# Optimization experiments

Hardware: AMD Instinct MI355X
Metric: run time of the kernel (lower is better)

Reference implementation:

```python
import jax, jax.numpy as jnp
import numpy as np

STRIDES = [8, 16, 32]
FMP = [(320, 320), (160, 160), (80, 80)]  # H,W per level for 2560x2560 input
NUM_CLASSES = 80
TOPK = 1000
CONF_THRESH = 0.05
NMS_THRESH = 0.6
CLASS_OFFSET = 8192.0  # > max coordinate; separates classes for class-aware NMS


def setup_inputs() -> dict:
    key = jax.random.key(0)
    ks = jax.random.split(key, 9)
    d = {}
    for i, (h, w) in enumerate(FMP):
        M = h * w
        d[f"obj{i}"] = jax.random.normal(ks[3 * i], (M, 1), jnp.float32)
        d[f"cls{i}"] = jax.random.normal(ks[3 * i + 1], (M, NUM_CLASSES), jnp.float32)
        d[f"reg{i}"] = jax.random.normal(ks[3 * i + 2], (M, 4), jnp.float32) * 0.5
    return d


def _anchors(level):
    h, w = FMP[level]
    ys, xs = jnp.meshgrid(jnp.arange(h), jnp.arange(w), indexing='ij')
    xy = jnp.stack([xs, ys], axis=-1).reshape(-1, 2).astype(jnp.float32) + 0.5
    return xy * STRIDES[level]  # [M, 2]


def _decode_boxes(anchors, regs, stride):
    ctr = anchors + regs[..., :2] * stride
    wh = jnp.exp(regs[..., 2:]) * stride
    return jnp.concatenate([ctr - 0.5 * wh, ctr + 0.5 * wh], axis=-1)


def _level_topk(obj, cls_, reg, level):
    # fused score: sqrt(sigmoid(obj) * sigmoid(cls)), flattened over [M*C]
    scores = jnp.sqrt(jax.nn.sigmoid(obj) * jax.nn.sigmoid(cls_)).reshape(-1)
    top_s, top_i = jax.lax.top_k(scores, TOPK)
    valid = top_s > CONF_THRESH  # original filters; we mask (jit-friendly)
    anchor_idx = top_i // NUM_CLASSES
    labels = top_i % NUM_CLASSES
    boxes = _decode_boxes(_anchors(level)[anchor_idx], reg[anchor_idx], STRIDES[level])
    return top_s, labels, boxes, valid


def _iou_matrix(b):
    # b: [N,4] -> pairwise IoU [N,N]
    area = (b[:, 2] - b[:, 0]) * (b[:, 3] - b[:, 1])
    lt = jnp.maximum(b[:, None, :2], b[None, :, :2])
    rb = jnp.minimum(b[:, None, 2:], b[None, :, 2:])
    wh = jnp.clip(rb - lt, 0.0)
    inter = wh[..., 0] * wh[..., 1]
    return inter / (area[:, None] + area[None, :] - inter + 1e-9)


def _multiclass_nms(boxes, scores, labels, valid):
    N = scores.shape[0]
    order = jnp.argsort(-scores)
    boxes = boxes[order]
    scores = scores[order]
    labels = labels[order]
    valid = valid[order]
    # class-aware NMS via coordinate offset trick
    off_boxes = boxes + (labels.astype(jnp.float32) * CLASS_OFFSET)[:, None]
    iou = _iou_matrix(off_boxes)
    idx = jnp.arange(N)

    def body(i, keep):
        sup = (iou[i] > NMS_THRESH) & (idx > i)
        return jnp.where(keep[i], keep & ~sup, keep)

    keep = jax.lax.fori_loop(0, N, body, valid)
    return boxes, scores, labels, keep


def reference(obj0, cls0, reg0, obj1, cls1, reg1, obj2, cls2, reg2):
    objs, clss, regs = [obj0, obj1, obj2], [cls0, cls1, cls2], [reg0, reg1, reg2]
    S, L, B, V = [], [], [], []
    for lvl in range(3):
        s, l, b, v = _level_topk(objs[lvl], clss[lvl], regs[lvl], lvl)
        S.append(s); L.append(l); B.append(b); V.append(v)
    scores = jnp.concatenate(S)
    labels = jnp.concatenate(L)
    boxes = jnp.concatenate(B)
    valid = jnp.concatenate(V)
    boxes, scores, labels, keep = _multiclass_nms(boxes, scores, labels, valid)
    return boxes, scores, labels, keep
```

## Files before the change

kernel.cpp:

```cpp
#include <hip/hip_runtime.h>

typedef unsigned int u32;
typedef unsigned long long u64;

#define NCLS 80
#define NTOT 3000
#define CAND_CAP 4096
#define NBLK 525

#define WS_HIST   0
#define WS_CNT    3072
#define WS_DONEA  3200
#define WS_DONEB  3328
#define WS_DONEC  3456
#define WS_CAND   4096
#define WS_SEL    102400

#define PB_HALF    0x3F000000u
#define PB_QUARTER 0x3E800000u

__device__ __forceinline__ float sigm(float x) {
#pragma clang fp contract(off)
    return 1.0f / (1.0f + expf(-x));
}

__device__ __forceinline__ u32 cload32(const u32* p) {
    return __hip_atomic_load(p, __ATOMIC_RELAXED, __HIP_MEMORY_SCOPE_AGENT);
}
__device__ __forceinline__ u64 cload64(const u64* p) {
    return __hip_atomic_load(p, __ATOMIC_RELAXED, __HIP_MEMORY_SCOPE_AGENT);
}
__device__ __forceinline__ void cstore64(u64* p, u64 v) {
    __hip_atomic_store(p, v, __ATOMIC_RELAXED, __HIP_MEMORY_SCOPE_AGENT);
}
__device__ __forceinline__ void arrive(u32* flag) {
    __hip_atomic_fetch_add(flag, 1u, __ATOMIC_RELEASE, __HIP_MEMORY_SCOPE_AGENT);
}
__device__ __forceinline__ void wait_for(u32* flag, u32 target) {
    int it = 0;
    while (__hip_atomic_load(flag, __ATOMIC_RELAXED, __HIP_MEMORY_SCOPE_AGENT) < target
           && it++ < (1 << 24)) {
        __builtin_amdgcn_s_sleep(8);
    }
    (void)__hip_atomic_load(flag, __ATOMIC_ACQUIRE, __HIP_MEMORY_SCOPE_AGENT);
}

__device__ __forceinline__ void block_map(int b, int& L, int& m0) {
    if (b < 400)      { L = 0; m0 = b * 256; }
    else if (b < 500) { L = 1; m0 = (b - 400) * 256; }
    else              { L = 2; m0 = (b - 500) * 256; }
}

__global__ __launch_bounds__(256) void fused_kernel(
    const float* __restrict__ o0, const float* __restrict__ c0, const float* __restrict__ r0,
    const float* __restrict__ o1, const float* __restrict__ c1, const float* __restrict__ r1,
    const float* __restrict__ o2, const float* __restrict__ c2, const float* __restrict__ r2,
    float* __restrict__ out,
    u32* __restrict__ whist, u32* __restrict__ wcnt,
    u32* __restrict__ doneA, u32* __restrict__ doneB, u32* __restrict__ doneC,
    u64* __restrict__ wcand, u64* __restrict__ wsel) {
#pragma clang fp contract(off)
    __shared__ u64 smem64[4096];
    int tid = threadIdx.x;
    int b = (int)blockIdx.x;
    u32 lane = (u32)(tid & 63);
    int L, m0; block_map(b, L, m0);
    const float* obj = (L == 0) ? o0 : ((L == 1) ? o1 : o2);
    const float* cls = (L == 0) ? c0 : ((L == 1) ? c1 : c2);
    const float4* cls4 = (const float4*)cls;

    {
        u32* h = (u32*)smem64;
        u32* alist = h + 8 * 257;
        float* slist = (float*)(alist + 256);
        u32* nshp = (u32*)(slist + 256);
        for (int k = tid; k < 8 * 257; k += 256) h[k] = 0u;
        if (tid == 0) *nshp = 0u;
        __syncthreads();
        float so = sigm(obj[m0 + tid]);
        bool pass = __float_as_uint(so) >= PB_HALF;
        u64 mask = __ballot(pass);
        u32 pc = (u32)__popcll(mask);
        u32 wbase = 0;
        if (lane == 0 && pc) wbase = atomicAdd(nshp, pc);
        wbase = (u32)__shfl((int)wbase, 0);
        if (pass) {
            u32 off = (u32)__popcll(mask & ((1ull << lane) - 1ull));
            alist[wbase + off] = (u32)tid;
            slist[wbase + off] = so;
        }
        __syncthreads();
        int n = (int)*nshp;
        u32 rep = (u32)(tid & 7);
        for (int i = tid; i < n * 20; i += 256) {
            int j = i / 20, k = i - j * 20;
            int a = m0 + (int)alist[j];
            float soj = slist[j];
            float4 v = cls4[a * 20 + k];
            float vv[4] = {v.x, v.y, v.z, v.w};
#pragma unroll
            for (int q = 0; q < 4; ++q) {
                float p = soj * sigm(vv[q]);
                u32 pb = __float_as_uint(p);
                if (pb >= PB_HALF) {
                    u32 bin = min((pb >> 15) - 0x7E00u, 255u);
                    atomicAdd(&h[rep * 257 + bin], 1u);
                }
            }
        }
        __syncthreads();
        if (tid < 256) {
            u32 s = 0;
            for (int r = 0; r < 8; ++r) s += h[r * 257 + tid];
            if (s) atomicAdd(&whist[L * 256 + tid], s);
        }
    }
    __syncthreads();
    if (tid == 0) { arrive(doneA); wait_for(doneA, NBLK); }
    __syncthreads();

    {
        u32* sh = (u32*)smem64;
        u32* alist = sh + 256;
        float* slist = (float*)(alist + 256);
        int* cutbin = (int*)(slist + 256);
        u32* thrsh = (u32*)(cutbin + 1);
        u32* nshp = thrsh + 1;
        if (tid == 0) { *cutbin = -1; *nshp = 0u; }
        sh[tid] = cload32(&whist[L * 256 + tid]);
        __syncthreads();
        for (int off = 1; off < 256; off <<= 1) {
            u32 v = (tid + off < 256) ? sh[tid + off] : 0u;
            __syncthreads();
            sh[tid] += v;
            __syncthreads();
        }
        if (sh[tid] >= 1000u) atomicMax(cutbin, tid);
        __syncthreads();
        if (tid == 0) {
            *thrsh = (*cutbin >= 0) ? (PB_HALF + ((u32)*cutbin << 15)) - 0x8000u
                                    : PB_QUARTER;
        }
        __syncthreads();
        u32 thr = *thrsh;
        float so = sigm(obj[m0 + tid]);
        bool pass = __float_as_uint(so) >= thr;
        u64 mask = __ballot(pass);
        u32 pc = (u32)__popcll(mask);
        u32 wbase = 0;
        if (lane == 0 && pc) wbase = atomicAdd(nshp, pc);
        wbase = (u32)__shfl((int)wbase, 0);
        if (pass) {
            u32 off = (u32)__popcll(mask & ((1ull << lane) - 1ull));
            alist[wbase + off] = (u32)tid;
            slist[wbase + off] = so;
        }
        __syncthreads();
        int n = (int)*nshp;
        for (int i = tid; i < n * 20; i += 256) {
            int j = i / 20, k = i - j * 20;
            int a = m0 + (int)alist[j];
            float soj = slist[j];
            float4 v = cls4[a * 20 + k];
            float vv[4] = {v.x, v.y, v.z, v.w};
#pragma unroll
            for (int q = 0; q < 4; ++q) {
                float p = soj * sigm(vv[q]);
                u32 pb = __float_as_uint(p);
                bool emit = (pb >= thr);
                u64 em = __ballot(emit);
                if (em) {
                    u32 cw = (u32)__popcll(em);
                    u32 base = 0;
                    if (lane == 0) base = atomicAdd(&wcnt[L], cw);
                    base = (u32)__shfl((int)base, 0);
                    if (emit) {
                        u32 slot = base + (u32)__popcll(em & ((1ull << lane) - 1ull));
                        if (slot < CAND_CAP) {
                            float s = sqrtf(p);
                            u32 sb = __float_as_uint(s);
                            u32 idx = (u32)(a * NCLS + (k * 4 + q));
                            cstore64(&wcand[L * CAND_CAP + slot],
                                     ((u64)(sb ^ 0xFFFFFFFFu) << 32) | idx);
                        }
                    }
                }
            }
        }
    }
    __syncthreads();
    if (tid == 0) arrive(doneB);

    if (b < 48) {
        if (tid == 0) wait_for(doneB, NBLK);
        __syncthreads();
        u64* s = smem64;
        int RL = b >> 4, part = b & 15;
        int n = (int)min(cload32(&wcnt[RL]), (u32)CAND_CAP);
        if (part * 256 < n) {
            for (int j = tid; j < n; j += 256) s[j] = cload64(&wcand[RL * CAND_CAP + j]);
            __syncthreads();
            int i = part * 256 + tid;
            if (i < n) {
                u64 mykey = s[i];
                int rank = 0;
#pragma unroll 4
                for (int j = 0; j < n; ++j) rank += (s[j] < mykey);
                if (rank < 1000) cstore64(&wsel[RL * 1000 + rank], mykey);
            }
        }
        __syncthreads();
        if (tid == 0) arrive(doneC);
        return;
    }

    if (b >= 128) return;
    {
        int c = b - 48;
        u64* k = smem64;
        u64* ckey = smem64 + 3000;
        u32* cidx = (u32*)(smem64 + 3256);
        u32* ncp = (u32*)(smem64 + 3384);
        if (tid == 0) { *ncp = 0u; wait_for(doneC, 48); }
        __syncthreads();
        for (int i = tid; i < NTOT; i += 256) {
            u64 S = cload64(&wsel[i]);
            u64 key = (S & 0xFFFFFFFF00000000ull) | (u32)i;
            k[i] = key;
            u32 idx = (u32)S;
            if ((int)(idx % NCLS) == c) {
                u32 p = atomicAdd(ncp, 1u);
                if (p < 256) { ckey[p] = key; cidx[p] = idx; }
            }
        }
        __syncthreads();
        int nc = (int)min(*ncp, 256u);
        int g = -1, r = 0;
        u32 myidx = 0;
        u64 mykey = 0;
        if (tid < nc) {
            mykey = ckey[tid];
            myidx = cidx[tid];
            for (int j = 0; j < nc; ++j) r += (ckey[j] < mykey);
            int t = (int)(u32)mykey;
            int ML = t / 1000;
            g = t - ML * 1000;
            for (int O = 0; O < 3; ++O) {
                if (O == ML) continue;
                int lo = 0, hi = 1000;
                while (lo < hi) {
                    int mid = (lo + hi) >> 1;
                    if (k[O * 1000 + mid] < mykey) lo = mid + 1; else hi = mid;
                }
                g += lo;
            }
        }
        __syncthreads();
        u32* garr = (u32*)smem64;
        u32* invp = (u32*)(smem64 + 64);
        float* bx = (float*)(smem64 + 512);
        if (tid < nc) {
            garr[tid] = (u32)g;
            invp[r] = (u32)tid;
            int t = (int)(u32)mykey;
            int ML = t / 1000;
            u32 bits = (u32)(mykey >> 32) ^ 0xFFFFFFFFu;
            float score = __uint_as_float(bits);
            int m = (int)(myidx / NCLS);
            int w = (ML == 0) ? 320 : ((ML == 1) ? 160 : 80);
            float st = (ML == 0) ? 8.0f : ((ML == 1) ? 16.0f : 32.0f);
            const float* reg = (ML == 0) ? r0 : ((ML == 1) ? r1 : r2);
            int x = m % w, y = m / w;
            float rv0 = reg[m * 4 + 0], rv1 = reg[m * 4 + 1];
            float rv2 = reg[m * 4 + 2], rv3 = reg[m * 4 + 3];
            float ax = ((float)x + 0.5f) * st;
            float ay = ((float)y + 0.5f) * st;
            float cx = ax + rv0 * st;
            float cy = ay + rv1 * st;
            float bw = expf(rv2) * st;
            float bh = expf(rv3) * st;
            float hx = 0.5f * bw, hy = 0.5f * bh;
            float x1 = cx - hx, y1 = cy - hy, x2 = cx + hx, y2 = cy + hy;
            out[g * 4 + 0] = x1; out[g * 4 + 1] = y1;
            out[g * 4 + 2] = x2; out[g * 4 + 3] = y2;
            out[12000 + g] = score;
            out[15000 + g] = (float)c;
            float off = (float)c * 8192.0f;
            bx[tid * 4 + 0] = x1 + off; bx[tid * 4 + 1] = y1 + off;
            bx[tid * 4 + 2] = x2 + off; bx[tid * 4 + 3] = y2 + off;
        }
        __syncthreads();
        if (tid < 64) {
            int K = (nc + 63) >> 6;
            u32 alive = 0;
            for (int kk = 0; kk < K; ++kk) {
                int p = tid + (kk << 6);
                if (p < nc) {
                    u32 bits = (u32)(ckey[invp[p]] >> 32) ^ 0xFFFFFFFFu;
                    if (__uint_as_float(bits) > 0.05f) alive |= (1u << kk);
                }
            }
            for (int a = 0; a < nc; ++a) {
                u32 owner = (u32)__shfl((int)alive, a & 63);
                if ((owner >> (a >> 6)) & 1u) {
                    int ra = (int)invp[a];
                    float a0 = bx[ra * 4 + 0], a1 = bx[ra * 4 + 1];
                    float a2 = bx[ra * 4 + 2], a3 = bx[ra * 4 + 3];
                    float areaA = (a2 - a0) * (a3 - a1);
                    for (int kk = (a >> 6); kk < K; ++kk) {
                        int p = tid + (kk << 6);
                        if (p > a && p < nc && ((alive >> kk) & 1u)) {
                            int rp = (int)invp[p];
                            float b0 = bx[rp * 4 + 0], b1 = bx[rp * 4 + 1];
                            float b2 = bx[rp * 4 + 2], b3 = bx[rp * 4 + 3];
                            float areaB = (b2 - b0) * (b3 - b1);
                            float ltx = fmaxf(a0, b0), lty = fmaxf(a1, b1);
                            float rbx = fminf(a2, b2), rby = fminf(a3, b3);
                            float wx = fmaxf(rbx - ltx, 0.0f), wy = fmaxf(rby - lty, 0.0f);
                            float inter = wx * wy;
                            float denom = ((areaA + areaB) - inter) + 1e-9f;
                            float iou = inter / denom;
                            if (iou > 0.6f) alive &= ~(1u << kk);
                        }
                    }
                }
            }
            for (int kk = 0; kk < K; ++kk) {
                int p = tid + (kk << 6);
                if (p < nc)
                    out[18000 + garr[invp[p]]] = ((alive >> kk) & 1u) ? 1.0f : 0.0f;
            }
        }
    }
}

extern "C" void kernel_launch(void* const* d_in, const int* in_sizes, int n_in,
                              void* d_out, int out_size, void* d_ws, size_t ws_size,
                              hipStream_t stream) {
    const float* obj0 = (const float*)d_in[0];
    const float* cls0 = (const float*)d_in[1];
    const float* reg0 = (const float*)d_in[2];
    const float* obj1 = (const float*)d_in[3];
    const float* cls1 = (const float*)d_in[4];
    const float* reg1 = (const float*)d_in[5];
    const float* obj2 = (const float*)d_in[6];
    const float* cls2 = (const float*)d_in[7];
    const float* reg2 = (const float*)d_in[8];
    float* out = (float*)d_out;
    char* ws = (char*)d_ws;

    u32* hist  = (u32*)(ws + WS_HIST);
    u32* cnt   = (u32*)(ws + WS_CNT);
    u32* doneA = (u32*)(ws + WS_DONEA);
    u32* doneB = (u32*)(ws + WS_DONEB);
    u32* doneC = (u32*)(ws + WS_DONEC);
    u64* cand  = (u64*)(ws + WS_CAND);
    u64* sel   = (u64*)(ws + WS_SEL);

    hipMemsetAsync(ws, 0, 4096, stream);
    fused_kernel<<<NBLK, 256, 0, stream>>>(obj0, cls0, reg0, obj1, cls1, reg1,
                                           obj2, cls2, reg2, out,
                                           hist, cnt, doneA, doneB, doneC,
                                           cand, sel);
}
```

Measured before the change: 235.0 us.

## Split fused persistent kernel into three launches replacing grid-wide spin barriers

Replaces the single 525-block persistent kernel, which used global atomic arrive/wait barriers between the histogram, filter and rank/NMS phases, with three separate kernel launches that use stream ordering instead. The histogram and filter phases now map 128 anchors per block across 1050 blocks, so more blocks run with less shared memory each, and their inner loops are unrolled. The spin-wait sleep interval for the remaining intra-kernel barrier is shortened. The cost is extra launch overhead and a second read of obj/cls data from a fresh launch instead of reuse within one block.

```diff
diff --git a/kernel.cpp b/kernel.cpp
--- a/kernel.cpp
+++ b/kernel.cpp
@@ -6,12 +6,9 @@
 #define NCLS 80
 #define NTOT 3000
 #define CAND_CAP 4096
-#define NBLK 525
 
 #define WS_HIST   0
 #define WS_CNT    3072
-#define WS_DONEA  3200
-#define WS_DONEB  3328
 #define WS_DONEC  3456
 #define WS_CAND   4096
 #define WS_SEL    102400
@@ -24,9 +21,6 @@
     return 1.0f / (1.0f + expf(-x));
 }
 
-__device__ __forceinline__ u32 cload32(const u32* p) {
-    return __hip_atomic_load(p, __ATOMIC_RELAXED, __HIP_MEMORY_SCOPE_AGENT);
-}
 __device__ __forceinline__ u64 cload64(const u64* p) {
     return __hip_atomic_load(p, __ATOMIC_RELAXED, __HIP_MEMORY_SCOPE_AGENT);
 }
@@ -40,165 +34,178 @@
     int it = 0;
     while (__hip_atomic_load(flag, __ATOMIC_RELAXED, __HIP_MEMORY_SCOPE_AGENT) < target
            && it++ < (1 << 24)) {
-        __builtin_amdgcn_s_sleep(8);
+        __builtin_amdgcn_s_sleep(2);
     }
     (void)__hip_atomic_load(flag, __ATOMIC_ACQUIRE, __HIP_MEMORY_SCOPE_AGENT);
 }
 
-__device__ __forceinline__ void block_map(int b, int& L, int& m0) {
-    if (b < 400)      { L = 0; m0 = b * 256; }
-    else if (b < 500) { L = 1; m0 = (b - 400) * 256; }
-    else              { L = 2; m0 = (b - 500) * 256; }
-}
-
-__global__ __launch_bounds__(256) void fused_kernel(
-    const float* __restrict__ o0, const float* __restrict__ c0, const float* __restrict__ r0,
-    const float* __restrict__ o1, const float* __restrict__ c1, const float* __restrict__ r1,
-    const float* __restrict__ o2, const float* __restrict__ c2, const float* __restrict__ r2,
-    float* __restrict__ out,
-    u32* __restrict__ whist, u32* __restrict__ wcnt,
-    u32* __restrict__ doneA, u32* __restrict__ doneB, u32* __restrict__ doneC,
-    u64* __restrict__ wcand, u64* __restrict__ wsel) {
+__device__ __forceinline__ void block_map128(int b, int& L, int& m0) {
+    if (b < 800)       { L = 0; m0 = b * 128; }
+    else if (b < 1000) { L = 1; m0 = (b - 800) * 128; }
+    else               { L = 2; m0 = (b - 1000) * 128; }
+}
+
+__global__ __launch_bounds__(256) void hist_kernel(
+    const float* __restrict__ o0, const float* __restrict__ c0,
+    const float* __restrict__ o1, const float* __restrict__ c1,
+    const float* __restrict__ o2, const float* __restrict__ c2,
+    u32* __restrict__ whist) {
 #pragma clang fp contract(off)
-    __shared__ u64 smem64[4096];
+    __shared__ u32 h[8 * 257];
+    __shared__ u32 alist[128];
+    __shared__ float slist[128];
+    __shared__ u32 nsh;
     int tid = threadIdx.x;
     int b = (int)blockIdx.x;
-    u32 lane = (u32)(tid & 63);
-    int L, m0; block_map(b, L, m0);
+    int L, m0; block_map128(b, L, m0);
     const float* obj = (L == 0) ? o0 : ((L == 1) ? o1 : o2);
     const float* cls = (L == 0) ? c0 : ((L == 1) ? c1 : c2);
     const float4* cls4 = (const float4*)cls;
-
-    {
-        u32* h = (u32*)smem64;
-        u32* alist = h + 8 * 257;
-        float* slist = (float*)(alist + 256);
-        u32* nshp = (u32*)(slist + 256);
-        for (int k = tid; k < 8 * 257; k += 256) h[k] = 0u;
-        if (tid == 0) *nshp = 0u;
-        __syncthreads();
+    for (int k = tid; k < 8 * 257; k += 256) h[k] = 0u;
+    if (tid == 0) nsh = 0u;
+    __syncthreads();
+    if (tid < 128) {
+        u32 lane = (u32)(tid & 63);
         float so = sigm(obj[m0 + tid]);
         bool pass = __float_as_uint(so) >= PB_HALF;
         u64 mask = __ballot(pass);
         u32 pc = (u32)__popcll(mask);
         u32 wbase = 0;
-        if (lane == 0 && pc) wbase = atomicAdd(nshp, pc);
+        if (lane == 0 && pc) wbase = atomicAdd(&nsh, pc);
         wbase = (u32)__shfl((int)wbase, 0);
         if (pass) {
             u32 off = (u32)__popcll(mask & ((1ull << lane) - 1ull));
             alist[wbase + off] = (u32)tid;
             slist[wbase + off] = so;
         }
+    }
+    __syncthreads();
+    int n = (int)nsh;
+    u32 rep = (u32)(tid & 7);
+#pragma unroll 4
+    for (int i = tid; i < n * 20; i += 256) {
+        int j = i / 20, k = i - j * 20;
+        int a = m0 + (int)alist[j];
+        float soj = slist[j];
+        float4 v = cls4[a * 20 + k];
+        float vv[4] = {v.x, v.y, v.z, v.w};
+#pragma unroll
+        for (int q = 0; q < 4; ++q) {
+            float p = soj * sigm(vv[q]);
+            u32 pb = __float_as_uint(p);
+            if (pb >= PB_HALF) {
+                u32 bin = min((pb >> 15) - 0x7E00u, 255u);
+                atomicAdd(&h[rep * 257 + bin], 1u);
+            }
+        }
+    }
+    __syncthreads();
+    if (tid < 256) {
+        u32 s = 0;
+        for (int r = 0; r < 8; ++r) s += h[r * 257 + tid];
+        if (s) atomicAdd(&whist[L * 256 + tid], s);
+    }
+}
+
+__global__ __launch_bounds__(256) void filter_kernel(
+    const float* __restrict__ o0, const float* __restrict__ c0,
+    const float* __restrict__ o1, const float* __restrict__ c1,
+    const float* __restrict__ o2, const float* __restrict__ c2,
+    const u32* __restrict__ whist, u32* __restrict__ wcnt, u64* __restrict__ wcand) {
+#pragma clang fp contract(off)
+    __shared__ u32 sh[256];
+    __shared__ u32 alist[128];
+    __shared__ float slist[128];
+    __shared__ int cutbin;
+    __shared__ u32 thrsh, nsh;
+    int tid = threadIdx.x;
+    int b = (int)blockIdx.x;
+    u32 lane = (u32)(tid & 63);
+    int L, m0; block_map128(b, L, m0);
+    const float* obj = (L == 0) ? o0 : ((L == 1) ? o1 : o2);
+    const float* cls = (L == 0) ? c0 : ((L == 1) ? c1 : c2);
+    const float4* cls4 = (const float4*)cls;
+    if (tid == 0) { cutbin = -1; nsh = 0u; }
+    sh[tid] = whist[L * 256 + tid];
+    __syncthreads();
+    for (int off = 1; off < 256; off <<= 1) {
+        u32 v = (tid + off < 256) ? sh[tid + off] : 0u;
         __syncthreads();
-        int n = (int)*nshp;
-        u32 rep = (u32)(tid & 7);
-        for (int i = tid; i < n * 20; i += 256) {
-            int j = i / 20, k = i - j * 20;
-            int a = m0 + (int)alist[j];
-            float soj = slist[j];
-            float4 v = cls4[a * 20 + k];
-            float vv[4] = {v.x, v.y, v.z, v.w};
-#pragma unroll
-            for (int q = 0; q < 4; ++q) {
-                float p = soj * sigm(vv[q]);
-                u32 pb = __float_as_uint(p);
-                if (pb >= PB_HALF) {
-                    u32 bin = min((pb >> 15) - 0x7E00u, 255u);
-                    atomicAdd(&h[rep * 257 + bin], 1u);
-                }
-            }
-        }
+        sh[tid] += v;
         __syncthreads();
-        if (tid < 256) {
-            u32 s = 0;
-            for (int r = 0; r < 8; ++r) s += h[r * 257 + tid];
-            if (s) atomicAdd(&whist[L * 256 + tid], s);
-        }
-    }
-    __syncthreads();
-    if (tid == 0) { arrive(doneA); wait_for(doneA, NBLK); }
-    __syncthreads();
-
-    {
-        u32* sh = (u32*)smem64;
-        u32* alist = sh + 256;
-        float* slist = (float*)(alist + 256);
-        int* cutbin = (int*)(slist + 256);
-        u32* thrsh = (u32*)(cutbin + 1);
-        u32* nshp = thrsh + 1;
-        if (tid == 0) { *cutbin = -1; *nshp = 0u; }
-        sh[tid] = cload32(&whist[L * 256 + tid]);
-        __syncthreads();
-        for (int off = 1; off < 256; off <<= 1) {
-            u32 v = (tid + off < 256) ? sh[tid + off] : 0u;
-            __syncthreads();
-            sh[tid] += v;
-            __syncthreads();
-        }
-        if (sh[tid] >= 1000u) atomicMax(cutbin, tid);
-        __syncthreads();
-        if (tid == 0) {
-            *thrsh = (*cutbin >= 0) ? (PB_HALF + ((u32)*cutbin << 15)) - 0x8000u
-                                    : PB_QUARTER;
-        }
-        __syncthreads();
-        u32 thr = *thrsh;
+    }
+    if (sh[tid] >= 1000u) atomicMax(&cutbin, tid);
+    __syncthreads();
+    if (tid == 0) {
+        thrsh = (cutbin >= 0) ? (PB_HALF + ((u32)cutbin << 15)) - 0x8000u
+                              : PB_QUARTER;
+    }
+    __syncthreads();
+    u32 thr = thrsh;
+    if (tid < 128) {
         float so = sigm(obj[m0 + tid]);
         bool pass = __float_as_uint(so) >= thr;
         u64 mask = __ballot(pass);
         u32 pc = (u32)__popcll(mask);
         u32 wbase = 0;
-        if (lane == 0 && pc) wbase = atomicAdd(nshp, pc);
+        if (lane == 0 && pc) wbase = atomicAdd(&nsh, pc);
         wbase = (u32)__shfl((int)wbase, 0);
         if (pass) {
             u32 off = (u32)__popcll(mask & ((1ull << lane) - 1ull));
             alist[wbase + off] = (u32)tid;
             slist[wbase + off] = so;
         }
-        __syncthreads();
-        int n = (int)*nshp;
-        for (int i = tid; i < n * 20; i += 256) {
-            int j = i / 20, k = i - j * 20;
-            int a = m0 + (int)alist[j];
-            float soj = slist[j];
-            float4 v = cls4[a * 20 + k];
-            float vv[4] = {v.x, v.y, v.z, v.w};
+    }
+    __syncthreads();
+    int n = (int)nsh;
+#pragma unroll 4
+    for (int i = tid; i < n * 20; i += 256) {
+        int j = i / 20, k = i - j * 20;
+        int a = m0 + (int)alist[j];
+        float soj = slist[j];
+        float4 v = cls4[a * 20 + k];
+        float vv[4] = {v.x, v.y, v.z, v.w};
 #pragma unroll
-            for (int q = 0; q < 4; ++q) {
-                float p = soj * sigm(vv[q]);
-                u32 pb = __float_as_uint(p);
-                bool emit = (pb >= thr);
-                u64 em = __ballot(emit);
-                if (em) {
-                    u32 cw = (u32)__popcll(em);
-                    u32 base = 0;
-                    if (lane == 0) base = atomicAdd(&wcnt[L], cw);
-                    base = (u32)__shfl((int)base, 0);
-                    if (emit) {
-                        u32 slot = base + (u32)__popcll(em & ((1ull << lane) - 1ull));
-                        if (slot < CAND_CAP) {
-                            float s = sqrtf(p);
-                            u32 sb = __float_as_uint(s);
-                            u32 idx = (u32)(a * NCLS + (k * 4 + q));
-                            cstore64(&wcand[L * CAND_CAP + slot],
-                                     ((u64)(sb ^ 0xFFFFFFFFu) << 32) | idx);
-                        }
+        for (int q = 0; q < 4; ++q) {
+            float p = soj * sigm(vv[q]);
+            u32 pb = __float_as_uint(p);
+            bool emit = (pb >= thr);
+            u64 em = __ballot(emit);
+            if (em) {
+                u32 cw = (u32)__popcll(em);
+                u32 base = 0;
+                if (lane == 0) base = atomicAdd(&wcnt[L], cw);
+                base = (u32)__shfl((int)base, 0);
+                if (emit) {
+                    u32 slot = base + (u32)__popcll(em & ((1ull << lane) - 1ull));
+                    if (slot < CAND_CAP) {
+                        float s = sqrtf(p);
+                        u32 sb = __float_as_uint(s);
+                        u32 idx = (u32)(a * NCLS + (k * 4 + q));
+                        wcand[L * CAND_CAP + slot] = ((u64)(sb ^ 0xFFFFFFFFu) << 32) | idx;
                     }
                 }
             }
         }
     }
-    __syncthreads();
-    if (tid == 0) arrive(doneB);
+}
+
+__global__ __launch_bounds__(256) void rank_nms_kernel(
+    const u32* __restrict__ wcnt, const u64* __restrict__ wcand,
+    u64* __restrict__ wsel, u32* __restrict__ doneC,
+    const float* __restrict__ r0, const float* __restrict__ r1,
+    const float* __restrict__ r2, float* __restrict__ out) {
+#pragma clang fp contract(off)
+    __shared__ u64 smem64[4096];
+    int tid = threadIdx.x;
+    int b = (int)blockIdx.x;
 
     if (b < 48) {
-        if (tid == 0) wait_for(doneB, NBLK);
-        __syncthreads();
         u64* s = smem64;
         int RL = b >> 4, part = b & 15;
-        int n = (int)min(cload32(&wcnt[RL]), (u32)CAND_CAP);
+        int n = (int)min(wcnt[RL], (u32)CAND_CAP);
         if (part * 256 < n) {
-            for (int j = tid; j < n; j += 256) s[j] = cload64(&wcand[RL * CAND_CAP + j]);
+            for (int j = tid; j < n; j += 256) s[j] = wcand[RL * CAND_CAP + j];
             __syncthreads();
             int i = part * 256 + tid;
             if (i < n) {
@@ -214,122 +221,119 @@
         return;
     }
 
-    if (b >= 128) return;
-    {
-        int c = b - 48;
-        u64* k = smem64;
-        u64* ckey = smem64 + 3000;
-        u32* cidx = (u32*)(smem64 + 3256);
-        u32* ncp = (u32*)(smem64 + 3384);
-        if (tid == 0) { *ncp = 0u; wait_for(doneC, 48); }
-        __syncthreads();
-        for (int i = tid; i < NTOT; i += 256) {
-            u64 S = cload64(&wsel[i]);
-            u64 key = (S & 0xFFFFFFFF00000000ull) | (u32)i;
-            k[i] = key;
-            u32 idx = (u32)S;
-            if ((int)(idx % NCLS) == c) {
-                u32 p = atomicAdd(ncp, 1u);
-                if (p < 256) { ckey[p] = key; cidx[p] = idx; }
-            }
-        }
-        __syncthreads();
-        int nc = (int)min(*ncp, 256u);
-        int g = -1, r = 0;
-        u32 myidx = 0;
-        u64 mykey = 0;
-        if (tid < nc) {
-            mykey = ckey[tid];
-            myidx = cidx[tid];
-            for (int j = 0; j < nc; ++j) r += (ckey[j] < mykey);
-            int t = (int)(u32)mykey;
-            int ML = t / 1000;
-            g = t - ML * 1000;
-            for (int O = 0; O < 3; ++O) {
-                if (O == ML) continue;
-                int lo = 0, hi = 1000;
-                while (lo < hi) {
-                    int mid = (lo + hi) >> 1;
-                    if (k[O * 1000 + mid] < mykey) lo = mid + 1; else hi = mid;
-                }
-                g += lo;
-            }
-        }
-        __syncthreads();
-        u32* garr = (u32*)smem64;
-        u32* invp = (u32*)(smem64 + 64);
-        float* bx = (float*)(smem64 + 512);
-        if (tid < nc) {
-            garr[tid] = (u32)g;
-            invp[r] = (u32)tid;
-            int t = (int)(u32)mykey;
-            int ML = t / 1000;
-            u32 bits = (u32)(mykey >> 32) ^ 0xFFFFFFFFu;
-            float score = __uint_as_float(bits);
-            int m = (int)(myidx / NCLS);
-            int w = (ML == 0) ? 320 : ((ML == 1) ? 160 : 80);
-            float st = (ML == 0) ? 8.0f : ((ML == 1) ? 16.0f : 32.0f);
-            const float* reg = (ML == 0) ? r0 : ((ML == 1) ? r1 : r2);
-            int x = m % w, y = m / w;
-            float rv0 = reg[m * 4 + 0], rv1 = reg[m * 4 + 1];
-            float rv2 = reg[m * 4 + 2], rv3 = reg[m * 4 + 3];
-            float ax = ((float)x + 0.5f) * st;
-            float ay = ((float)y + 0.5f) * st;
-            float cx = ax + rv0 * st;
-            float cy = ay + rv1 * st;
-            float bw = expf(rv2) * st;
-            float bh = expf(rv3) * st;
-            float hx = 0.5f * bw, hy = 0.5f * bh;
-            float x1 = cx - hx, y1 = cy - hy, x2 = cx + hx, y2 = cy + hy;
-            out[g * 4 + 0] = x1; out[g * 4 + 1] = y1;
-            out[g * 4 + 2] = x2; out[g * 4 + 3] = y2;
-            out[12000 + g] = score;
-            out[15000 + g] = (float)c;
-            float off = (float)c * 8192.0f;
-            bx[tid * 4 + 0] = x1 + off; bx[tid * 4 + 1] = y1 + off;
-            bx[tid * 4 + 2] = x2 + off; bx[tid * 4 + 3] = y2 + off;
-        }
-        __syncthreads();
-        if (tid < 64) {
-            int K = (nc + 63) >> 6;
-            u32 alive = 0;
-            for (int kk = 0; kk < K; ++kk) {
-                int p = tid + (kk << 6);
-                if (p < nc) {
-                    u32 bits = (u32)(ckey[invp[p]] >> 32) ^ 0xFFFFFFFFu;
-                    if (__uint_as_float(bits) > 0.05f) alive |= (1u << kk);
-                }
-            }
-            for (int a = 0; a < nc; ++a) {
-                u32 owner = (u32)__shfl((int)alive, a & 63);
-                if ((owner >> (a >> 6)) & 1u) {
-                    int ra = (int)invp[a];
-                    float a0 = bx[ra * 4 + 0], a1 = bx[ra * 4 + 1];
-                    float a2 = bx[ra * 4 + 2], a3 = bx[ra * 4 + 3];
-                    float areaA = (a2 - a0) * (a3 - a1);
-                    for (int kk = (a >> 6); kk < K; ++kk) {
-                        int p = tid + (kk << 6);
-                        if (p > a && p < nc && ((alive >> kk) & 1u)) {
-                            int rp = (int)invp[p];
-                            float b0 = bx[rp * 4 + 0], b1 = bx[rp * 4 + 1];
-                            float b2 = bx[rp * 4 + 2], b3 = bx[rp * 4 + 3];
-                            float areaB = (b2 - b0) * (b3 - b1);
-                            float ltx = fmaxf(a0, b0), lty = fmaxf(a1, b1);
-                            float rbx = fminf(a2, b2), rby = fminf(a3, b3);
-                            float wx = fmaxf(rbx - ltx, 0.0f), wy = fmaxf(rby - lty, 0.0f);
-                            float inter = wx * wy;
-                            float denom = ((areaA + areaB) - inter) + 1e-9f;
-                            float iou = inter / denom;
-                            if (iou > 0.6f) alive &= ~(1u << kk);
-                        }
+    int c = b - 48;
+    u64* k = smem64;
+    u64* ckey = smem64 + 3000;
+    u32* cidx = (u32*)(smem64 + 3256);
+    u32* ncp = (u32*)(smem64 + 3384);
+    if (tid == 0) { *ncp = 0u; wait_for(doneC, 48); }
+    __syncthreads();
+    for (int i = tid; i < NTOT; i += 256) {
+        u64 S = cload64(&wsel[i]);
+        u64 key = (S & 0xFFFFFFFF00000000ull) | (u32)i;
+        k[i] = key;
+        u32 idx = (u32)S;
+        if ((int)(idx % NCLS) == c) {
+            u32 p = atomicAdd(ncp, 1u);
+            if (p < 256) { ckey[p] = key; cidx[p] = idx; }
+        }
+    }
+    __syncthreads();
+    int nc = (int)min(*ncp, 256u);
+    int g = -1, r = 0;
+    u32 myidx = 0;
+    u64 mykey = 0;
+    if (tid < nc) {
+        mykey = ckey[tid];
+        myidx = cidx[tid];
+        for (int j = 0; j < nc; ++j) r += (ckey[j] < mykey);
+        int t = (int)(u32)mykey;
+        int ML = t / 1000;
+        g = t - ML * 1000;
+        for (int O = 0; O < 3; ++O) {
+            if (O == ML) continue;
+            int lo = 0, hi = 1000;
+            while (lo < hi) {
+                int mid = (lo + hi) >> 1;
+                if (k[O * 1000 + mid] < mykey) lo = mid + 1; else hi = mid;
+            }
+            g += lo;
+        }
+    }
+    __syncthreads();
+    u32* garr = (u32*)smem64;
+    u32* invp = (u32*)(smem64 + 64);
+    float* bx = (float*)(smem64 + 512);
+    if (tid < nc) {
+        garr[tid] = (u32)g;
+        invp[r] = (u32)tid;
+        int t = (int)(u32)mykey;
+        int ML = t / 1000;
+        u32 bits = (u32)(mykey >> 32) ^ 0xFFFFFFFFu;
+        float score = __uint_as_float(bits);
+        int m = (int)(myidx / NCLS);
+        int w = (ML == 0) ? 320 : ((ML == 1) ? 160 : 80);
+        float st = (ML == 0) ? 8.0f : ((ML == 1) ? 16.0f : 32.0f);
+        const float* reg = (ML == 0) ? r0 : ((ML == 1) ? r1 : r2);
+        int x = m % w, y = m / w;
+        float rv0 = reg[m * 4 + 0], rv1 = reg[m * 4 + 1];
+        float rv2 = reg[m * 4 + 2], rv3 = reg[m * 4 + 3];
+        float ax = ((float)x + 0.5f) * st;
+        float ay = ((float)y + 0.5f) * st;
+        float cx = ax + rv0 * st;
+        float cy = ay + rv1 * st;
+        float bw = expf(rv2) * st;
+        float bh = expf(rv3) * st;
+        float hx = 0.5f * bw, hy = 0.5f * bh;
+        float x1 = cx - hx, y1 = cy - hy, x2 = cx + hx, y2 = cy + hy;
+        out[g * 4 + 0] = x1; out[g * 4 + 1] = y1;
+        out[g * 4 + 2] = x2; out[g * 4 + 3] = y2;
+        out[12000 + g] = score;
+        out[15000 + g] = (float)c;
+        float off = (float)c * 8192.0f;
+        bx[tid * 4 + 0] = x1 + off; bx[tid * 4 + 1] = y1 + off;
+        bx[tid * 4 + 2] = x2 + off; bx[tid * 4 + 3] = y2 + off;
+    }
+    __syncthreads();
+    if (tid < 64) {
+        int K = (nc + 63) >> 6;
+        u32 alive = 0;
+        for (int kk = 0; kk < K; ++kk) {
+            int p = tid + (kk << 6);
+            if (p < nc) {
+                u32 bits = (u32)(ckey[invp[p]] >> 32) ^ 0xFFFFFFFFu;
+                if (__uint_as_float(bits) > 0.05f) alive |= (1u << kk);
+            }
+        }
+        for (int a = 0; a < nc; ++a) {
+            u32 owner = (u32)__shfl((int)alive, a & 63);
+            if ((owner >> (a >> 6)) & 1u) {
+                int ra = (int)invp[a];
+                float a0 = bx[ra * 4 + 0], a1 = bx[ra * 4 + 1];
+                float a2 = bx[ra * 4 + 2], a3 = bx[ra * 4 + 3];
+                float areaA = (a2 - a0) * (a3 - a1);
+                for (int kk = (a >> 6); kk < K; ++kk) {
+                    int p = tid + (kk << 6);
+                    if (p > a && p < nc && ((alive >> kk) & 1u)) {
+                        int rp = (int)invp[p];
+                        float b0 = bx[rp * 4 + 0], b1 = bx[rp * 4 + 1];
+                        float b2 = bx[rp * 4 + 2], b3 = bx[rp * 4 + 3];
+                        float areaB = (b2 - b0) * (b3 - b1);
+                        float ltx = fmaxf(a0, b0), lty = fmaxf(a1, b1);
+                        float rbx = fminf(a2, b2), rby = fminf(a3, b3);
+                        float wx = fmaxf(rbx - ltx, 0.0f), wy = fmaxf(rby - lty, 0.0f);
+                        float inter = wx * wy;
+                        float denom = ((areaA + areaB) - inter) + 1e-9f;
+                        float iou = inter / denom;
+                        if (iou > 0.6f) alive &= ~(1u << kk);
                     }
                 }
             }
-            for (int kk = 0; kk < K; ++kk) {
-                int p = tid + (kk << 6);
-                if (p < nc)
-                    out[18000 + garr[invp[p]]] = ((alive >> kk) & 1u) ? 1.0f : 0.0f;
-            }
+        }
+        for (int kk = 0; kk < K; ++kk) {
+            int p = tid + (kk << 6);
+            if (p < nc)
+                out[18000 + garr[invp[p]]] = ((alive >> kk) & 1u) ? 1.0f : 0.0f;
         }
     }
 }
@@ -351,15 +355,14 @@
 
     u32* hist  = (u32*)(ws + WS_HIST);
     u32* cnt   = (u32*)(ws + WS_CNT);
-    u32* doneA = (u32*)(ws + WS_DONEA);
-    u32* doneB = (u32*)(ws + WS_DONEB);
     u32* doneC = (u32*)(ws + WS_DONEC);
     u64* cand  = (u64*)(ws + WS_CAND);
     u64* sel   = (u64*)(ws + WS_SEL);
 
     hipMemsetAsync(ws, 0, 4096, stream);
-    fused_kernel<<<NBLK, 256, 0, stream>>>(obj0, cls0, reg0, obj1, cls1, reg1,
-                                           obj2, cls2, reg2, out,
-                                           hist, cnt, doneA, doneB, doneC,
-                                           cand, sel);
-}
+    hist_kernel<<<1050, 256, 0, stream>>>(obj0, cls0, obj1, cls1, obj2, cls2, hist);
+    filter_kernel<<<1050, 256, 0, stream>>>(obj0, cls0, obj1, cls1, obj2, cls2,
+                                            hist, cnt, cand);
+    rank_nms_kernel<<<128, 256, 0, stream>>>(cnt, cand, sel, doneC,
+                                             reg0, reg1, reg2, out);
+}
```

Result: faster. 201.0 us (-14.5%).
